# Performance work log

Measured on AMD Instinct MI355X. Metric: run time of the kernel, lower is better.

## Reference

```python
import jax, jax.numpy as jnp
import numpy as np

B, C, D, H = 4, 1024, 768, 12      # batch, seq_len(>512 long-doc), hidden, heads
E, K, S, V, P = 32, 2, 24, 8, 512  # entities, mentions/entity, sents, virtual nodes, ht pairs
NT = 256                            # node type embedding dim
EMB, BLK, NL = 768, 64, 97          # emb_size, block_size, num_labels
OFFSET = 1


def setup_inputs() -> dict:
    key = jax.random.key(0)
    ks = jax.random.split(key, 13)
    return {
        "sequence_output": jax.random.normal(ks[0], (B, C, D), jnp.float32),
        "attention": jax.random.uniform(ks[1], (B, H, C, C), jnp.float32),
        "entity_pos": jax.random.randint(ks[2], (B, E, K), 0, C - 2),
        "sent_pos": jax.random.randint(ks[3], (B, S), 0, C - 2),
        "virtual_pos": jax.random.randint(ks[4], (B, V), 0, C - 2),
        "hts": jax.random.randint(ks[5], (B, P, 2), 0, E),
        "node_type_emb": jax.random.normal(ks[6], (B, E, NT), jnp.float32) * 0.02,
        "W_head": jax.random.normal(ks[7], (2 * D + NT, EMB), jnp.float32) * 0.02,
        "b_head": jnp.zeros((EMB,), jnp.float32),
        "W_tail": jax.random.normal(ks[8], (2 * D + NT, EMB), jnp.float32) * 0.02,
        "b_tail": jnp.zeros((EMB,), jnp.float32),
        "W_bil": jax.random.normal(ks[9], (EMB * BLK, NL), jnp.float32) * 0.02,
        "b_bil": jnp.zeros((NL,), jnp.float32),
    }


def reference(sequence_output, attention, entity_pos, sent_pos, virtual_pos, hts,
              node_type_emb, W_head, b_head, W_tail, b_tail, W_bil, b_bil):
    # --- get_mention_embed / get_entity_embed: gather mention-start rows ---
    idx = entity_pos + OFFSET                      # [B,E,K] token index of each mention start
    flat = idx.reshape(B, E * K)                   # mention order matches torch double loop
    mention_embed = jnp.take_along_axis(sequence_output, flat[:, :, None], axis=1)  # [B,E*K,D]
    entity_embed = jax.nn.logsumexp(mention_embed.reshape(B, E, K, D), axis=2)      # [B,E,D]

    # --- get_sent_embed / get_virtual_embed: single-row gathers ---
    sent_embed = jnp.take_along_axis(sequence_output, (sent_pos + OFFSET)[:, :, None], axis=1)      # [B,S,D]
    virtual_embed = jnp.take_along_axis(sequence_output, (virtual_pos + OFFSET)[:, :, None], axis=1)  # [B,V,D]

    # --- get_rss: localized-context pooling over attention ---
    att_t = attention.transpose(0, 2, 1, 3)        # [B,C,H,C] so we gather query rows
    e_att = jnp.take_along_axis(att_t, flat[:, :, None, None], axis=1)  # [B,E*K,H,C]
    e_att = e_att.reshape(B, E, K, H, C).mean(axis=2)                   # [B,E,H,C] mean over mentions
    h_att = jnp.take_along_axis(e_att, hts[:, :, 0][:, :, None, None], axis=1)  # [B,P,H,C]
    t_att = jnp.take_along_axis(e_att, hts[:, :, 1][:, :, None, None], axis=1)  # [B,P,H,C]
    ht_att = (h_att * t_att).mean(axis=2)                               # [B,P,C] mean over heads
    ht_att = ht_att / (ht_att.sum(axis=-1, keepdims=True) + 1e-5)
    rs = jnp.einsum('bld,brl->brd', sequence_output, ht_att)            # [B,P,D]

    # --- get_pair_entity_embed on entity hidden state (entity_embed + node-type emb) ---
    ent_hidden = jnp.concatenate([entity_embed, node_type_emb], axis=-1)          # [B,E,D+NT]
    s_emb = jnp.take_along_axis(ent_hidden, hts[:, :, 0][:, :, None], axis=1)     # [B,P,D+NT]
    t_emb = jnp.take_along_axis(ent_hidden, hts[:, :, 1][:, :, None], axis=1)

    # --- head/tail extractors + grouped bilinear classifier ---
    hs = jnp.tanh(jnp.concatenate([s_emb, rs], axis=-1) @ W_head + b_head)  # [B,P,EMB]
    ts = jnp.tanh(jnp.concatenate([t_emb, rs], axis=-1) @ W_tail + b_tail)
    b1 = hs.reshape(B, P, EMB // BLK, BLK)
    b2 = ts.reshape(B, P, EMB // BLK, BLK)
    bl = (b1[..., :, None] * b2[..., None, :]).reshape(B, P, EMB * BLK)     # [B,P,EMB*BLK]
    logits = bl @ W_bil + b_bil                                             # [B,P,NL]
    return (logits, mention_embed, sent_embed, virtual_embed)
```

## Files before the change

### kernel.cpp

```cpp
#include <hip/hip_runtime.h>

#define B_   4
#define C_   1024
#define D_   768
#define H_   12
#define E_   32
#define K_   2
#define S_   24
#define V_   8
#define P_   512
#define NT_  256
#define EMB_ 768
#define BLK_ 64
#define NL_  97
#define DNT_ 1024
#define KHT_ 1792
#define KBIL_ 49152
#define NPAD_ 128
#define NGIC_ 24

typedef __bf16 bf16x8 __attribute__((ext_vector_type(8)));
typedef float  f32x4  __attribute__((ext_vector_type(4)));

__device__ __forceinline__ float b2f(unsigned short u) {
    return (float)__builtin_bit_cast(__bf16, u);
}
__device__ __forceinline__ unsigned short f2b(float f) {
    return __builtin_bit_cast(unsigned short, (__bf16)f);
}
__device__ __forceinline__ float ld_in(const void* p, size_t i, int isf) {
    return isf ? ((const float*)p)[i] : b2f(((const unsigned short*)p)[i]);
}
__device__ __forceinline__ void st_out(void* p, size_t i, float v, int isf) {
    if (isf) ((float*)p)[i] = v;
    else     ((unsigned short*)p)[i] = f2b(v);
}
__device__ __forceinline__ int probe_isf(const void* seq) {
    unsigned short u = ((const unsigned short*)seq)[2 * (threadIdx.x & 63)];
    int huge = !(fabsf(b2f(u)) <= 1e10f);
    unsigned long long zb = __ballot(u == 0);
    return __any(huge) || (__popcll(zb) > 56);
}

#define PREP_GATHER 256
#define PREP_EATT   (PREP_GATHER + B_*E_*H_)
#define PREP_TSEQ   (PREP_EATT + 768)
#define PREP_TW     (PREP_TSEQ + 672)
#define PREP_TBIL   (PREP_TW + 768)

__global__ __launch_bounds__(256) void k_prep(
    const void* __restrict__ seq, const void* __restrict__ att,
    const int* __restrict__ epos, const int* __restrict__ spos,
    const int* __restrict__ vpos, const void* __restrict__ ntype,
    const void* __restrict__ Wh, const void* __restrict__ Wt_,
    const void* __restrict__ Wb,
    float* __restrict__ enth, unsigned short* __restrict__ e_att,
    unsigned short* __restrict__ seqT,
    unsigned short* __restrict__ WtH, unsigned short* __restrict__ WtT,
    unsigned short* __restrict__ WtB,
    void* __restrict__ outv, long long moff, long long soff, long long voff)
{
    __shared__ __align__(16) unsigned char smem[12544];
    int blk = blockIdx.x, tid = threadIdx.x;
    int isf = probe_isf(seq);
    if (blk < PREP_GATHER) {
        if (blk < B_ * E_) {
            int b = blk / E_, e = blk % E_;
            int i0 = epos[(b * E_ + e) * K_ + 0] + 1;
            int i1 = epos[(b * E_ + e) * K_ + 1] + 1;
            size_t r0 = ((size_t)b * C_ + i0) * D_;
            size_t r1 = ((size_t)b * C_ + i1) * D_;
            size_t m0 = (size_t)moff + ((size_t)(b * E_ * K_) + 2 * e) * D_;
            size_t m1 = m0 + D_;
            float* eh = enth + (size_t)(b * E_ + e) * DNT_;
            for (int d = tid; d < D_; d += 256) {
                float a = ld_in(seq, r0 + d, isf);
                float c = ld_in(seq, r1 + d, isf);
                st_out(outv, m0 + d, a, isf);
                st_out(outv, m1 + d, c, isf);
                float mx = fmaxf(a, c);
                eh[d] = mx + logf(expf(a - mx) + expf(c - mx));
            }
            size_t nt0 = (size_t)(b * E_ + e) * NT_;
            for (int j = tid; j < NT_; j += 256) eh[D_ + j] = ld_in(ntype, nt0 + j, isf);
        } else if (blk < B_ * E_ + B_ * S_) {
            int t = blk - B_ * E_; int b = t / S_, s = t % S_;
            int i = spos[b * S_ + s] + 1;
            size_t r = ((size_t)b * C_ + i) * D_;
            size_t o = (size_t)soff + (size_t)(b * S_ + s) * D_;
            for (int d = tid; d < D_; d += 256) st_out(outv, o + d, ld_in(seq, r + d, isf), isf);
        } else {
            int t = blk - B_ * E_ - B_ * S_; int b = t / V_, v = t % V_;
            int i = vpos[b * V_ + v] + 1;
            size_t r = ((size_t)b * C_ + i) * D_;
            size_t o = (size_t)voff + (size_t)(b * V_ + v) * D_;
            for (int d = tid; d < D_; d += 256) st_out(outv, o + d, ld_in(seq, r + d, isf), isf);
        }
    } else if (blk < PREP_EATT) {
        int t = blk - PREP_GATHER;
        int b = t / (E_ * H_); int r = t % (E_ * H_); int e = r / H_; int h = r % H_;
        int i0 = epos[(b * E_ + e) * K_ + 0] + 1;
        int i1 = epos[(b * E_ + e) * K_ + 1] + 1;
        size_t a0 = (((size_t)b * H_ + h) * C_ + i0) * C_;
        size_t a1 = (((size_t)b * H_ + h) * C_ + i1) * C_;
        unsigned short* o = e_att + (((size_t)(b * E_ + e)) * H_ + h) * C_;
        for (int c = tid; c < C_; c += 256)
            o[c] = f2b(0.5f * (ld_in(att, a0 + c, isf) + ld_in(att, a1 + c, isf)));
    } else if (blk < PREP_TSEQ) {
        int t = blk - PREP_EATT;
        int b = t / 192; int r = t % 192; int ct = r / 12; int dt = r % 12;
        typedef unsigned short row65[65];
        row65* tile = (row65*)smem;
        for (int idx = tid; idx < 4096; idx += 256) {
            int cc = idx >> 6, dd = idx & 63;
            tile[cc][dd] = f2b(ld_in(seq, ((size_t)b * C_ + ct * 64 + cc) * D_ + dt * 64 + dd, isf));
        }
        __syncthreads();
        for (int idx = tid; idx < 4096; idx += 256) {
            int dd = idx >> 6, cc = idx & 63;
            seqT[((size_t)b * D_ + dt * 64 + dd) * C_ + ct * 64 + cc] = tile[cc][dd];
        }
    } else if (blk < PREP_TW) {
        int t = blk - PREP_TSEQ;
        int mat = t / 336; int r = t % 336; int kt = r / 12; int nt = r % 12;
        const void* in = mat ? Wt_ : Wh;
        unsigned short* out = mat ? WtT : WtH;
        typedef unsigned short row65[65];
        row65* tile = (row65*)smem;
        for (int idx = tid; idx < 4096; idx += 256) {
            int kk = idx >> 6, nn = idx & 63;
            tile[kk][nn] = f2b(ld_in(in, ((size_t)kt * 64 + kk) * EMB_ + nt * 64 + nn, isf));
        }
        __syncthreads();
        for (int idx = tid; idx < 4096; idx += 256) {
            int nn = idx >> 6, kk = idx & 63;
            out[((size_t)nt * 64 + nn) * KHT_ + kt * 64 + kk] = tile[kk][nn];
        }
    } else {
        int t = blk - PREP_TW;
        int g = t >> 6, i = t & 63;
        unsigned short* raw = (unsigned short*)smem;
        size_t src0 = ((size_t)g * 4096 + (size_t)i * 64) * NL_;
        for (int idx = tid; idx < 64 * NL_; idx += 256)
            raw[idx] = f2b(ld_in(Wb, src0 + idx, isf));
        __syncthreads();
        for (int idx = tid; idx < 8192; idx += 256) {
            int w = idx >> 10, o = idx & 1023;
            int jh = o >> 9, q = (o >> 7) & 3, l15 = (o >> 3) & 15, e = o & 7;
            int j = jh * 32 + q * 8 + e;
            int n = w * 16 + l15;
            unsigned short v = (n < NL_) ? raw[j * NL_ + n] : (unsigned short)0;
            WtB[(((size_t)(g * 8 + w) * 64 + i) << 10) + o] = v;
        }
    }
}

__global__ __launch_bounds__(256) void k_mid(
    const unsigned short* __restrict__ e_att, const float* __restrict__ enth,
    const int* __restrict__ hts,
    unsigned short* __restrict__ htb,
    unsigned short* __restrict__ Xh, unsigned short* __restrict__ Xt)
{
    __shared__ float red[4];
    int blk = blockIdx.x, tid = threadIdx.x;
    if (blk < B_ * P_) {
        int b = blk >> 9;
        int he = hts[blk * 2 + 0], te = hts[blk * 2 + 1];
        const unsigned short* ph = e_att + (size_t)(b * E_ + he) * H_ * C_;
        const unsigned short* pt = e_att + (size_t)(b * E_ + te) * H_ * C_;
        float v[4]; float ls = 0.f;
        for (int ci = 0; ci < 4; ci++) {
            int c = tid + (ci << 8);
            float acc = 0.f;
#pragma unroll
            for (int h = 0; h < H_; h++) acc += b2f(ph[h * C_ + c]) * b2f(pt[h * C_ + c]);
            acc *= (1.0f / (float)H_);
            v[ci] = acc; ls += acc;
        }
        for (int off = 32; off > 0; off >>= 1) ls += __shfl_down(ls, off, 64);
        if ((tid & 63) == 0) red[tid >> 6] = ls;
        __syncthreads();
        float inv = 1.0f / (red[0] + red[1] + red[2] + red[3] + 1e-5f);
        for (int ci = 0; ci < 4; ci++)
            htb[((size_t)blk << 10) + tid + (ci << 8)] = f2b(v[ci] * inv);
    } else {
        int m = blk - B_ * P_; int b = m >> 9;
        int eh = hts[m * 2 + 0], et = hts[m * 2 + 1];
        const float* sh = enth + (size_t)(b * E_ + eh) * DNT_;
        const float* st = enth + (size_t)(b * E_ + et) * DNT_;
        for (int k = tid; k < DNT_; k += 256) {
            Xh[(size_t)m * KHT_ + k] = f2b(sh[k]);
            Xt[(size_t)m * KHT_ + k] = f2b(st[k]);
        }
    }
}

__global__ __launch_bounds__(256) void k_gemm(
    const unsigned short* __restrict__ A0, const unsigned short* __restrict__ A1,
    const unsigned short* __restrict__ B0, const unsigned short* __restrict__ B1,
    long long lda, long long ldb, long long sAz, long long sBz,
    int nsteps, int zmode,
    const void* __restrict__ bias0, const void* __restrict__ bias1,
    unsigned short* __restrict__ oY0, unsigned short* __restrict__ oY1,
    unsigned short* __restrict__ oX1, unsigned short* __restrict__ oX2,
    const void* __restrict__ seq)
{
    int n0 = blockIdx.x * 64, m0 = blockIdx.y * 64, z = blockIdx.z;
    const unsigned short* Ab; const unsigned short* Bb;
    unsigned short* oY = nullptr; const void* bias = nullptr;
    if (zmode == 0) {
        Ab = A0 + (size_t)z * sAz; Bb = B0 + (size_t)z * sBz;
    } else {
        Ab = z ? A1 : A0; Bb = z ? B1 : B0;
        oY = z ? oY1 : oY0; bias = z ? bias1 : bias0;
    }
    __shared__ __align__(16) unsigned short a_lds[64][40];
    __shared__ __align__(16) unsigned short b_lds[64][40];
    int tid = threadIdx.x, lane = tid & 63, w = tid >> 6;
    int wm = (w >> 1) * 32, wn = (w & 1) * 32, q = lane >> 4, l15 = lane & 15;
    f32x4 acc00 = {0.f,0.f,0.f,0.f}, acc01 = acc00, acc10 = acc00, acc11 = acc00;
    int srow = tid >> 2, sch = (tid & 3) * 8;
    const unsigned short* pa = Ab + (size_t)(m0 + srow) * lda + sch;
    const unsigned short* pb = Bb + (size_t)(n0 + srow) * ldb + sch;
    int4 ra = *(const int4*)pa;
    int4 rb = *(const int4*)pb;
    for (int ks = 0; ks < nsteps; ks++) {
        __syncthreads();
        *(int4*)&a_lds[srow][sch] = ra;
        *(int4*)&b_lds[srow][sch] = rb;
        __syncthreads();
        if (ks + 1 < nsteps) {
            ra = *(const int4*)(pa + (size_t)(ks + 1) * 32);
            rb = *(const int4*)(pb + (size_t)(ks + 1) * 32);
        }
        bf16x8 a0 = *(const bf16x8*)&a_lds[wm + l15][q * 8];
        bf16x8 a1 = *(const bf16x8*)&a_lds[wm + 16 + l15][q * 8];
        bf16x8 b0 = *(const bf16x8*)&b_lds[wn + l15][q * 8];
        bf16x8 b1 = *(const bf16x8*)&b_lds[wn + 16 + l15][q * 8];
        acc00 = __builtin_amdgcn_mfma_f32_16x16x32_bf16(a0, b0, acc00, 0, 0, 0);
        acc01 = __builtin_amdgcn_mfma_f32_16x16x32_bf16(a0, b1, acc01, 0, 0, 0);
        acc10 = __builtin_amdgcn_mfma_f32_16x16x32_bf16(a1, b0, acc10, 0, 0, 0);
        acc11 = __builtin_amdgcn_mfma_f32_16x16x32_bf16(a1, b1, acc11, 0, 0, 0);
    }
    f32x4 accs[2][2] = {{acc00, acc01}, {acc10, acc11}};
    int isf = (zmode == 1) ? probe_isf(seq) : 0;
#pragma unroll
    for (int mt = 0; mt < 2; mt++)
#pragma unroll
        for (int nt = 0; nt < 2; nt++) {
            int gmb = m0 + wm + mt * 16 + q * 4;
            int gn  = n0 + wn + nt * 16 + l15;
            if (zmode == 0) {
#pragma unroll
                for (int r = 0; r < 4; r++) {
                    unsigned short v = f2b(accs[mt][nt][r]);
                    size_t o = (size_t)(z * P_ + gmb + r) * KHT_ + DNT_ + gn;
                    oX1[o] = v; oX2[o] = v;
                }
            } else {
                float bv = ld_in(bias, gn, isf);
#pragma unroll
                for (int r = 0; r < 4; r++)
                    oY[(size_t)(gmb + r) * EMB_ + gn] = f2b(tanhf(accs[mt][nt][r] + bv));
            }
        }
}

__global__ __launch_bounds__(512) void k_bil(
    const unsigned short* __restrict__ hsB, const unsigned short* __restrict__ tsB,
    const unsigned short* __restrict__ W2, float* __restrict__ logitsP)
{
    int bid = blockIdx.x;
    int lin = (bid & 7) * 96 + (bid >> 3);
    int mt  = lin & 31;
    int gic = lin >> 5;
    int g   = gic >> 1;
    int ic  = gic & 1;
    int m0  = mt * 64;

    int tid = threadIdx.x, lane = tid & 63, w = tid >> 6;
    int q = lane >> 4, l15 = lane & 15;
    int ns = w * 16;

    __shared__ __align__(16) unsigned short hsT[32][64];
    {
        int m = tid >> 3, i4 = (tid & 7) * 4;
        ushort4 hv = *(const ushort4*)&hsB[(size_t)(m0 + m) * EMB_ + g * 64 + ic * 32 + i4];
        hsT[i4 + 0][m] = hv.x; hsT[i4 + 1][m] = hv.y;
        hsT[i4 + 2][m] = hv.z; hsT[i4 + 3][m] = hv.w;
    }

    bf16x8 a[4][2];
#pragma unroll
    for (int ms = 0; ms < 4; ++ms)
#pragma unroll
        for (int jh = 0; jh < 2; ++jh)
            a[ms][jh] = *(const bf16x8*)&tsB[(size_t)(m0 + ms * 16 + l15) * EMB_
                                             + g * 64 + jh * 32 + q * 8];
    __syncthreads();

    const unsigned short* pw = W2 + (((size_t)(g * 8 + w) * 64 + ic * 32) << 10) + lane * 8;

    f32x4 acc[4];
#pragma unroll
    for (int ms = 0; ms < 4; ++ms) acc[ms] = (f32x4){0.f, 0.f, 0.f, 0.f};
    const f32x4 zf = {0.f, 0.f, 0.f, 0.f};

    bf16x8 w0a = *(const bf16x8*)(pw);
    bf16x8 w0b = *(const bf16x8*)(pw + 512);
    bf16x8 w1a = *(const bf16x8*)(pw + 1024);
    bf16x8 w1b = *(const bf16x8*)(pw + 1536);

#define BIL_STEP(ii, wa_, wb_)                                                             \
    do {                                                                                   \
        int ipre = (ii) + 2 <= 31 ? (ii) + 2 : 31;                                         \
        bf16x8 na = *(const bf16x8*)(pw + ((size_t)ipre << 10));                           \
        bf16x8 nb = *(const bf16x8*)(pw + ((size_t)ipre << 10) + 512);                     \
        f32x4 p[4];                                                                        \
        _Pragma("unroll")                                                                  \
        for (int ms = 0; ms < 4; ++ms) {                                                   \
            f32x4 t = __builtin_amdgcn_mfma_f32_16x16x32_bf16(a[ms][0], wa_, zf, 0, 0, 0); \
            p[ms]   = __builtin_amdgcn_mfma_f32_16x16x32_bf16(a[ms][1], wb_, t, 0, 0, 0);  \
        }                                                                                  \
        _Pragma("unroll")                                                                  \
        for (int ms = 0; ms < 4; ++ms) {                                                   \
            ushort4 hv = *(const ushort4*)&hsT[ii][ms * 16 + q * 4];                       \
            acc[ms][0] += b2f(hv.x) * p[ms][0];                                            \
            acc[ms][1] += b2f(hv.y) * p[ms][1];                                            \
            acc[ms][2] += b2f(hv.z) * p[ms][2];                                            \
            acc[ms][3] += b2f(hv.w) * p[ms][3];                                            \
        }                                                                                  \
        wa_ = na; wb_ = nb;                                                                \
    } while (0)

#pragma unroll 4
    for (int ii = 0; ii < 16; ++ii) {
        BIL_STEP(2 * ii,     w0a, w0b);
        BIL_STEP(2 * ii + 1, w1a, w1b);
    }
#undef BIL_STEP

    float* outp = logitsP + ((size_t)gic * (B_ * P_) + m0) * NPAD_ + ns + l15;
#pragma unroll
    for (int ms = 0; ms < 4; ++ms)
#pragma unroll
        for (int r = 0; r < 4; ++r)
            outp[(size_t)(ms * 16 + q * 4 + r) * NPAD_] = acc[ms][r];
}

__global__ __launch_bounds__(256) void k_fin(
    const float* __restrict__ logitsP, const void* __restrict__ b_bil,
    void* __restrict__ outv, const void* __restrict__ seq)
{
    int isf = probe_isf(seq);
    int idx = blockIdx.x * 256 + threadIdx.x;
    if (idx >= B_ * P_ * NL_) return;
    int m = idx / NL_, n = idx % NL_;
    float s = ld_in(b_bil, n, isf);
#pragma unroll
    for (int p = 0; p < NGIC_; ++p)
        s += logitsP[((size_t)p * (B_ * P_) + m) * NPAD_ + n];
    st_out(outv, idx, s, isf);
}

extern "C" void kernel_launch(void* const* d_in, const int* in_sizes, int n_in,
                              void* d_out, int out_size, void* d_ws, size_t ws_size,
                              hipStream_t stream)
{
    const void* seq    = d_in[0];
    const void* att    = d_in[1];
    const int*  epos   = (const int*)d_in[2];
    const int*  spos   = (const int*)d_in[3];
    const int*  vpos   = (const int*)d_in[4];
    const int*  hts    = (const int*)d_in[5];
    const void* ntype  = d_in[6];
    const void* W_head = d_in[7];
    const void* b_head = d_in[8];
    const void* W_tail = d_in[9];
    const void* b_tail = d_in[10];
    const void* W_bil  = d_in[11];
    const void* b_bil  = d_in[12];

    long long mention_off = (long long)B_ * P_ * NL_;
    long long sent_off    = mention_off + (long long)B_ * E_ * K_ * D_;
    long long virt_off    = sent_off + (long long)B_ * S_ * D_;

    char* p = (char*)d_ws;
    auto alloc = [&](size_t bytes) { void* r = (void*)p; p += (bytes + 255) & ~(size_t)255; return r; };
    unsigned short* e_att   = (unsigned short*)alloc((size_t)B_ * E_ * H_ * C_ * 2);
    unsigned short* htb     = (unsigned short*)alloc((size_t)B_ * P_ * C_ * 2);
    unsigned short* seqT    = (unsigned short*)alloc((size_t)B_ * D_ * C_ * 2);
    unsigned short* WtH     = (unsigned short*)alloc((size_t)EMB_ * KHT_ * 2);
    unsigned short* WtT     = (unsigned short*)alloc((size_t)EMB_ * KHT_ * 2);
    unsigned short* WtB     = (unsigned short*)alloc((size_t)NPAD_ * KBIL_ * 2);
    unsigned short* Xh      = (unsigned short*)alloc((size_t)B_ * P_ * KHT_ * 2);
    unsigned short* Xt      = (unsigned short*)alloc((size_t)B_ * P_ * KHT_ * 2);
    unsigned short* hsB     = (unsigned short*)alloc((size_t)B_ * P_ * EMB_ * 2);
    unsigned short* tsB     = (unsigned short*)alloc((size_t)B_ * P_ * EMB_ * 2);
    float*          logitsP = (float*)alloc((size_t)NGIC_ * B_ * P_ * NPAD_ * 4);
    float*          enth    = (float*)alloc((size_t)B_ * E_ * DNT_ * 4);

    dim3 blk(256);
    k_prep<<<PREP_TBIL, blk, 0, stream>>>(
        seq, att, epos, spos, vpos, ntype, W_head, W_tail, W_bil,
        enth, e_att, seqT, WtH, WtT, WtB,
        d_out, mention_off, sent_off, virt_off);
    k_mid<<<2 * B_ * P_, blk, 0, stream>>>(e_att, enth, hts, htb, Xh, Xt);
    k_gemm<<<dim3(EMB_ / 64, P_ / 64, B_), blk, 0, stream>>>(
        htb, nullptr, seqT, nullptr, C_, C_,
        (long long)P_ * C_, (long long)D_ * C_, C_ / 32, 0,
        nullptr, nullptr, nullptr, nullptr, Xh, Xt, seq);
    k_gemm<<<dim3(EMB_ / 64, (B_ * P_) / 64, 2), blk, 0, stream>>>(
        Xh, Xt, WtH, WtT, KHT_, KHT_, 0, 0, KHT_ / 32, 1,
        b_head, b_tail, hsB, tsB, nullptr, nullptr, seq);
    k_bil<<<dim3(768), dim3(512), 0, stream>>>(hsB, tsB, WtB, logitsP);
    k_fin<<<(B_ * P_ * NL_ + 255) / 256, blk, 0, stream>>>(logitsP, b_bil, d_out, seq);
}
```

Baseline: 387.6 us.

## Enlarge GEMM tiles to 128x64 with K=64 steps and deepen bilinear weight prefetch

The generic MFMA GEMM kernel now computes a 128x64 output tile per block with a 64-wide K step. Each wave holds a 4x2 grid of 16x16 accumulators, so there are more MFMAs per LDS load and half as many barrier iterations. Launch grids and step counts are adjusted to match. Separately, the bilinear kernel prefetches weights four steps ahead instead of two, to hide global load latency. The cost is more registers and LDS per block and half as many blocks, which may lower occupancy on the smaller GEMM.

```diff
diff --git a/kernel.cpp b/kernel.cpp
--- a/kernel.cpp
+++ b/kernel.cpp
@@ -205,7 +205,7 @@
     unsigned short* __restrict__ oX1, unsigned short* __restrict__ oX2,
     const void* __restrict__ seq)
 {
-    int n0 = blockIdx.x * 64, m0 = blockIdx.y * 64, z = blockIdx.z;
+    int n0 = blockIdx.x * 64, m0 = blockIdx.y * 128, z = blockIdx.z;
     const unsigned short* Ab; const unsigned short* Bb;
     unsigned short* oY = nullptr; const void* bias = nullptr;
     if (zmode == 0) {
@@ -214,46 +214,77 @@
         Ab = z ? A1 : A0; Bb = z ? B1 : B0;
         oY = z ? oY1 : oY0; bias = z ? bias1 : bias0;
     }
-    __shared__ __align__(16) unsigned short a_lds[64][40];
-    __shared__ __align__(16) unsigned short b_lds[64][40];
+    __shared__ __align__(16) unsigned short a_lds[128][72];
+    __shared__ __align__(16) unsigned short b_lds[64][72];
     int tid = threadIdx.x, lane = tid & 63, w = tid >> 6;
-    int wm = (w >> 1) * 32, wn = (w & 1) * 32, q = lane >> 4, l15 = lane & 15;
-    f32x4 acc00 = {0.f,0.f,0.f,0.f}, acc01 = acc00, acc10 = acc00, acc11 = acc00;
-    int srow = tid >> 2, sch = (tid & 3) * 8;
-    const unsigned short* pa = Ab + (size_t)(m0 + srow) * lda + sch;
-    const unsigned short* pb = Bb + (size_t)(n0 + srow) * ldb + sch;
-    int4 ra = *(const int4*)pa;
-    int4 rb = *(const int4*)pb;
+    int wm = (w >> 1) * 64, wn = (w & 1) * 32, q = lane >> 4, l15 = lane & 15;
+
+    f32x4 acc[4][2];
+#pragma unroll
+    for (int ms = 0; ms < 4; ++ms)
+#pragma unroll
+        for (int ns = 0; ns < 2; ++ns) acc[ms][ns] = (f32x4){0.f, 0.f, 0.f, 0.f};
+
+    int arow[4], acol[4], brow[2], bcol[2];
+    const unsigned short* pa[4]; const unsigned short* pb[2];
+#pragma unroll
+    for (int k2 = 0; k2 < 4; ++k2) {
+        int c = tid + k2 * 256;
+        arow[k2] = c >> 3; acol[k2] = (c & 7) * 8;
+        pa[k2] = Ab + (size_t)(m0 + arow[k2]) * lda + acol[k2];
+    }
+#pragma unroll
+    for (int k2 = 0; k2 < 2; ++k2) {
+        int c = tid + k2 * 256;
+        brow[k2] = c >> 3; bcol[k2] = (c & 7) * 8;
+        pb[k2] = Bb + (size_t)(n0 + brow[k2]) * ldb + bcol[k2];
+    }
+    int4 ra[4], rb[2];
+#pragma unroll
+    for (int k2 = 0; k2 < 4; ++k2) ra[k2] = *(const int4*)pa[k2];
+#pragma unroll
+    for (int k2 = 0; k2 < 2; ++k2) rb[k2] = *(const int4*)pb[k2];
+
     for (int ks = 0; ks < nsteps; ks++) {
         __syncthreads();
-        *(int4*)&a_lds[srow][sch] = ra;
-        *(int4*)&b_lds[srow][sch] = rb;
+#pragma unroll
+        for (int k2 = 0; k2 < 4; ++k2) *(int4*)&a_lds[arow[k2]][acol[k2]] = ra[k2];
+#pragma unroll
+        for (int k2 = 0; k2 < 2; ++k2) *(int4*)&b_lds[brow[k2]][bcol[k2]] = rb[k2];
         __syncthreads();
         if (ks + 1 < nsteps) {
-            ra = *(const int4*)(pa + (size_t)(ks + 1) * 32);
-            rb = *(const int4*)(pb + (size_t)(ks + 1) * 32);
-        }
-        bf16x8 a0 = *(const bf16x8*)&a_lds[wm + l15][q * 8];
-        bf16x8 a1 = *(const bf16x8*)&a_lds[wm + 16 + l15][q * 8];
-        bf16x8 b0 = *(const bf16x8*)&b_lds[wn + l15][q * 8];
-        bf16x8 b1 = *(const bf16x8*)&b_lds[wn + 16 + l15][q * 8];
-        acc00 = __builtin_amdgcn_mfma_f32_16x16x32_bf16(a0, b0, acc00, 0, 0, 0);
-        acc01 = __builtin_amdgcn_mfma_f32_16x16x32_bf16(a0, b1, acc01, 0, 0, 0);
-        acc10 = __builtin_amdgcn_mfma_f32_16x16x32_bf16(a1, b0, acc10, 0, 0, 0);
-        acc11 = __builtin_amdgcn_mfma_f32_16x16x32_bf16(a1, b1, acc11, 0, 0, 0);
-    }
-    f32x4 accs[2][2] = {{acc00, acc01}, {acc10, acc11}};
+#pragma unroll
+            for (int k2 = 0; k2 < 4; ++k2) ra[k2] = *(const int4*)(pa[k2] + (size_t)(ks + 1) * 64);
+#pragma unroll
+            for (int k2 = 0; k2 < 2; ++k2) rb[k2] = *(const int4*)(pb[k2] + (size_t)(ks + 1) * 64);
+        }
+#pragma unroll
+        for (int kk = 0; kk < 2; ++kk) {
+            bf16x8 af[4], bfr[2];
+#pragma unroll
+            for (int ms = 0; ms < 4; ++ms)
+                af[ms] = *(const bf16x8*)&a_lds[wm + ms * 16 + l15][kk * 32 + q * 8];
+#pragma unroll
+            for (int ns = 0; ns < 2; ++ns)
+                bfr[ns] = *(const bf16x8*)&b_lds[wn + ns * 16 + l15][kk * 32 + q * 8];
+#pragma unroll
+            for (int ms = 0; ms < 4; ++ms)
+#pragma unroll
+                for (int ns = 0; ns < 2; ++ns)
+                    acc[ms][ns] = __builtin_amdgcn_mfma_f32_16x16x32_bf16(af[ms], bfr[ns], acc[ms][ns], 0, 0, 0);
+        }
+    }
     int isf = (zmode == 1) ? probe_isf(seq) : 0;
 #pragma unroll
-    for (int mt = 0; mt < 2; mt++)
-#pragma unroll
-        for (int nt = 0; nt < 2; nt++) {
-            int gmb = m0 + wm + mt * 16 + q * 4;
-            int gn  = n0 + wn + nt * 16 + l15;
+    for (int ms = 0; ms < 4; ++ms)
+#pragma unroll
+        for (int ns = 0; ns < 2; ++ns) {
+            int gmb = m0 + wm + ms * 16 + q * 4;
+            int gn  = n0 + wn + ns * 16 + l15;
             if (zmode == 0) {
 #pragma unroll
                 for (int r = 0; r < 4; r++) {
-                    unsigned short v = f2b(accs[mt][nt][r]);
+                    unsigned short v = f2b(acc[ms][ns][r]);
                     size_t o = (size_t)(z * P_ + gmb + r) * KHT_ + DNT_ + gn;
                     oX1[o] = v; oX2[o] = v;
                 }
@@ -261,7 +292,7 @@
                 float bv = ld_in(bias, gn, isf);
 #pragma unroll
                 for (int r = 0; r < 4; r++)
-                    oY[(size_t)(gmb + r) * EMB_ + gn] = f2b(tanhf(accs[mt][nt][r] + bv));
+                    oY[(size_t)(gmb + r) * EMB_ + gn] = f2b(tanhf(acc[ms][ns][r] + bv));
             }
         }
 }
@@ -310,10 +341,14 @@
     bf16x8 w0b = *(const bf16x8*)(pw + 512);
     bf16x8 w1a = *(const bf16x8*)(pw + 1024);
     bf16x8 w1b = *(const bf16x8*)(pw + 1536);
+    bf16x8 w2a = *(const bf16x8*)(pw + 2048);
+    bf16x8 w2b = *(const bf16x8*)(pw + 2560);
+    bf16x8 w3a = *(const bf16x8*)(pw + 3072);
+    bf16x8 w3b = *(const bf16x8*)(pw + 3584);
 
 #define BIL_STEP(ii, wa_, wb_)                                                             \
     do {                                                                                   \
-        int ipre = (ii) + 2 <= 31 ? (ii) + 2 : 31;                                         \
+        int ipre = (ii) + 4 <= 31 ? (ii) + 4 : 31;                                         \
         bf16x8 na = *(const bf16x8*)(pw + ((size_t)ipre << 10));                           \
         bf16x8 nb = *(const bf16x8*)(pw + ((size_t)ipre << 10) + 512);                     \
         f32x4 p[4];                                                                        \
@@ -333,10 +368,12 @@
         wa_ = na; wb_ = nb;                                                                \
     } while (0)
 
-#pragma unroll 4
-    for (int ii = 0; ii < 16; ++ii) {
-        BIL_STEP(2 * ii,     w0a, w0b);
-        BIL_STEP(2 * ii + 1, w1a, w1b);
+#pragma unroll 2
+    for (int ii = 0; ii < 8; ++ii) {
+        BIL_STEP(4 * ii + 0, w0a, w0b);
+        BIL_STEP(4 * ii + 1, w1a, w1b);
+        BIL_STEP(4 * ii + 2, w2a, w2b);
+        BIL_STEP(4 * ii + 3, w3a, w3b);
     }
 #undef BIL_STEP
 
@@ -406,12 +443,12 @@
         enth, e_att, seqT, WtH, WtT, WtB,
         d_out, mention_off, sent_off, virt_off);
     k_mid<<<2 * B_ * P_, blk, 0, stream>>>(e_att, enth, hts, htb, Xh, Xt);
-    k_gemm<<<dim3(EMB_ / 64, P_ / 64, B_), blk, 0, stream>>>(
+    k_gemm<<<dim3(EMB_ / 64, P_ / 128, B_), blk, 0, stream>>>(
         htb, nullptr, seqT, nullptr, C_, C_,
-        (long long)P_ * C_, (long long)D_ * C_, C_ / 32, 0,
+        (long long)P_ * C_, (long long)D_ * C_, C_ / 64, 0,
         nullptr, nullptr, nullptr, nullptr, Xh, Xt, seq);
-    k_gemm<<<dim3(EMB_ / 64, (B_ * P_) / 64, 2), blk, 0, stream>>>(
-        Xh, Xt, WtH, WtT, KHT_, KHT_, 0, 0, KHT_ / 32, 1,
+    k_gemm<<<dim3(EMB_ / 64, (B_ * P_) / 128, 2), blk, 0, stream>>>(
+        Xh, Xt, WtH, WtT, KHT_, KHT_, 0, 0, KHT_ / 64, 1,
         b_head, b_tail, hsB, tsB, nullptr, nullptr, seq);
     k_bil<<<dim3(768), dim3(512), 0, stream>>>(hsB, tsB, WtB, logitsP);
     k_fin<<<(B_ * P_ * NL_ + 255) / 256, blk, 0, stream>>>(logitsP, b_bil, d_out, seq);
```

Result: slower. 475.6 us (+22.7%).
